# Optimization experiments

Measured on AMD Instinct MI355X. Metric: run time of the kernel, lower is better.

## Reference

```python
import jax, jax.numpy as jnp
import numpy as np

D = 1024      # config.input_dim
H = 16        # config.num_heads
EPS = 1e-6    # layernorm epsilon


def setup_inputs() -> dict:
    key = jax.random.key(0)
    ks = jax.random.split(key, 12)
    B, S = 4, 2048
    s = 1.0 / np.sqrt(D)
    return {
        "Q": jax.random.normal(ks[0], (B, S, D), jnp.float32),
        "K": jax.random.normal(ks[1], (B, S, D), jnp.float32),
        "V": jax.random.normal(ks[2], (B, S, D), jnp.float32),
        "Wq": jax.random.normal(ks[3], (D, D), jnp.float32) * s,
        "bq": jnp.zeros((D,), jnp.float32),
        "Wk": jax.random.normal(ks[4], (D, D), jnp.float32) * s,
        "bk": jnp.zeros((D,), jnp.float32),
        "Wv": jax.random.normal(ks[5], (D, D), jnp.float32) * s,
        "bv": jnp.zeros((D,), jnp.float32),
        "Wo": jax.random.normal(ks[6], (D, D), jnp.float32) * s,
        "bo": jnp.zeros((D,), jnp.float32),
        "gamma": jnp.ones((D,), jnp.float32),
        "beta": jnp.zeros((D,), jnp.float32),
    }


def _layernorm(x, gamma, beta):
    mu = jnp.mean(x, axis=-1, keepdims=True)
    var = jnp.mean(jnp.square(x - mu), axis=-1, keepdims=True)
    return (x - mu) * jax.lax.rsqrt(var + EPS) * gamma + beta


def reference(Q, K, V, Wq, bq, Wk, bk, Wv, bv, Wo, bo, gamma, beta):
    # Type == 'D': pre-norm projections, causal MHA (no 1/sqrt(d) scaling,
    # faithful to source), out projection, residual. Dropout = identity (eval).
    B, S, _ = Q.shape
    dh = D // H
    clone_Q = Q
    q = _layernorm(Q, gamma, beta) @ Wq + bq
    k = _layernorm(K, gamma, beta) @ Wk + bk
    v = _layernorm(V, gamma, beta) @ Wv + bv
    # [B, S, D] -> [B, H, S, dh]
    q = q.reshape(B, S, H, dh).transpose(0, 2, 1, 3)
    k = k.reshape(B, S, H, dh).transpose(0, 2, 1, 3)
    v = v.reshape(B, S, H, dh).transpose(0, 2, 1, 3)
    score = jnp.einsum("bhsd,bhtd->bhst", q, k)  # [B, H, S, S]
    causal = jnp.tril(jnp.ones((S, S), bool))
    score = jnp.where(causal, score, -jnp.inf)
    attn = jax.nn.softmax(score, axis=-1)
    out = jnp.einsum("bhst,bhtd->bhsd", attn, v)  # [B, H, S, dh]
    out = out.transpose(0, 2, 1, 3).reshape(B, S, D)
    return clone_Q + (out @ Wo + bo)
```

## Files before the change

kernel.cpp:

```cpp
#include <hip/hip_runtime.h>
#include <hip/hip_bf16.h>

typedef __attribute__((ext_vector_type(8))) __bf16 bf16x8;
typedef __attribute__((ext_vector_type(4))) float f32x4;

union BF8U { uint4 u; bf16x8 b; };

static __device__ __forceinline__ unsigned short f2bf(float f){
  __bf16 h = (__bf16)f;
  return *reinterpret_cast<unsigned short*>(&h);
}

static __device__ __forceinline__ bf16x8 ld_bf8(const unsigned short* p){
  BF8U u; u.u = *reinterpret_cast<const uint4*>(p); return u.b;
}

static __device__ __forceinline__ f32x4 mfma16(bf16x8 a, bf16x8 b, f32x4 c){
  return __builtin_amdgcn_mfma_f32_16x16x32_bf16(a, b, c, 0, 0, 0);
}

static __device__ __forceinline__ void gl_lds16(const unsigned short* g, unsigned short* l){
  __builtin_amdgcn_global_load_lds(
      (const __attribute__((address_space(1))) unsigned int*)g,
      (__attribute__((address_space(3))) unsigned int*)l, 16, 0, 0);
}

__global__ __launch_bounds__(256) void prep_kernel(
    const float* __restrict__ Q, const float* __restrict__ K, const float* __restrict__ V,
    const float* __restrict__ gamma, const float* __restrict__ beta,
    unsigned short* __restrict__ lnQ, unsigned short* __restrict__ lnK,
    unsigned short* __restrict__ lnV,
    const float* __restrict__ Wq, const float* __restrict__ Wk,
    const float* __restrict__ Wv, const float* __restrict__ Wo,
    unsigned short* __restrict__ WtQ, unsigned short* __restrict__ WtK,
    unsigned short* __restrict__ WtV, unsigned short* __restrict__ WtO)
{
  __shared__ __align__(16) unsigned short smem[64*72];
  const int bid = (int)blockIdx.x;
  const int t = threadIdx.x;
  if (bid < 24576){
    const int sel = bid >> 13;
    const int row = bid & 8191;
    const float* X = sel==0 ? Q : sel==1 ? K : V;
    unsigned short* out = sel==0 ? lnQ : sel==1 ? lnK : lnV;
    float* red = reinterpret_cast<float*>(smem);
    const float4 x = reinterpret_cast<const float4*>(X + (size_t)row*1024)[t];
    float s  = x.x + x.y + x.z + x.w;
    float ss = x.x*x.x + x.y*x.y + x.z*x.z + x.w*x.w;
    for (int off = 1; off < 64; off <<= 1){
      s  += __shfl_xor(s, off);
      ss += __shfl_xor(ss, off);
    }
    const int wv = t >> 6;
    if ((t & 63) == 0){ red[wv] = s; red[4 + wv] = ss; }
    __syncthreads();
    s  = red[0] + red[1] + red[2] + red[3];
    ss = red[4] + red[5] + red[6] + red[7];
    const float mu   = s * (1.0f/1024.0f);
    const float var  = ss * (1.0f/1024.0f) - mu*mu;
    const float rstd = rsqrtf(var + 1e-6f);
    const float4 gm = reinterpret_cast<const float4*>(gamma)[t];
    const float4 bt = reinterpret_cast<const float4*>(beta)[t];
    unsigned short pk[4];
    pk[0] = f2bf((x.x - mu)*rstd*gm.x + bt.x);
    pk[1] = f2bf((x.y - mu)*rstd*gm.y + bt.y);
    pk[2] = f2bf((x.z - mu)*rstd*gm.z + bt.z);
    pk[3] = f2bf((x.w - mu)*rstd*gm.w + bt.w);
    *reinterpret_cast<uint2*>(out + (size_t)row*1024 + t*4) = *reinterpret_cast<uint2*>(pk);
  } else {
    const int wid = bid - 24576;
    const int wsel = wid >> 8;
    const float* W = wsel==0 ? Wq : wsel==1 ? Wk : wsel==2 ? Wv : Wo;
    unsigned short* Wt = wsel==0 ? WtQ : wsel==1 ? WtK : wsel==2 ? WtV : WtO;
    unsigned short (*tile)[72] = reinterpret_cast<unsigned short(*)[72]>(smem);
    const int tb = wid & 255;
    const int bk = (tb >> 4) * 64;
    const int bn = (tb & 15) * 64;
    {
      const int kr = t >> 2, nc0 = (t & 3) * 16;
      const float4* src = reinterpret_cast<const float4*>(W + (size_t)(bk + kr)*1024 + bn + nc0);
      for (int q = 0; q < 4; ++q){
        float4 vv = src[q];
        tile[kr][nc0 + q*4 + 0] = f2bf(vv.x);
        tile[kr][nc0 + q*4 + 1] = f2bf(vv.y);
        tile[kr][nc0 + q*4 + 2] = f2bf(vv.z);
        tile[kr][nc0 + q*4 + 3] = f2bf(vv.w);
      }
    }
    __syncthreads();
    {
      const int nr = t >> 2, kc0 = (t & 3) * 16;
      unsigned short outv[16];
      for (int j = 0; j < 16; ++j) outv[j] = tile[kc0 + j][nr];
      uint4* dst = reinterpret_cast<uint4*>(Wt + (size_t)(bn + nr)*1024 + bk + kc0);
      dst[0] = reinterpret_cast<uint4*>(outv)[0];
      dst[1] = reinterpret_cast<uint4*>(outv)[1];
    }
  }
}

__global__ __launch_bounds__(256) void qkv_kernel(
    const unsigned short* __restrict__ lnQ, const unsigned short* __restrict__ lnK,
    const unsigned short* __restrict__ lnV,
    const unsigned short* __restrict__ WtQ, const unsigned short* __restrict__ WtK,
    const unsigned short* __restrict__ WtV,
    const float* __restrict__ bq, const float* __restrict__ bk,
    const float* __restrict__ bv,
    unsigned short* __restrict__ qb, unsigned short* __restrict__ kb,
    unsigned short* __restrict__ vtb)
{
  __shared__ unsigned short a_lds[128][64];
  __shared__ unsigned short b_lds[128][64];
  const int bid = (int)blockIdx.x;
  const int which = bid >> 9;
  const int inner = bid & 511;
  const unsigned short* A  = which==0 ? lnQ : which==1 ? lnK : lnV;
  const unsigned short* Bt = which==0 ? WtQ : which==1 ? WtK : WtV;
  const float* bias = which==0 ? bq : which==1 ? bk : bv;

  const int t = threadIdx.x;
  const int lane = t & 63;
  const int w = t >> 6;
  const int g = lane >> 4, c = lane & 15;
  const int bm = inner >> 3, bn = inner & 7;
  const int wr = w >> 1, wc = w & 1;
  const int row0 = bm * 128, col0 = bn * 128;

  f32x4 acc[4][4];
  const f32x4 fz = {0.f, 0.f, 0.f, 0.f};
  for (int i = 0; i < 4; ++i) for (int j = 0; j < 4; ++j) acc[i][j] = fz;

  for (int kb_ = 0; kb_ < 1024; kb_ += 64){
    for (int i = 0; i < 4; ++i){
      const int cid = t + i*256;
      const int r = cid >> 3, ch = cid & 7;
      const int chs = (ch ^ (r & 7)) * 8;
      gl_lds16(&A [(size_t)(row0 + r)*1024 + kb_ + chs], &a_lds[0][0] + cid*8);
      gl_lds16(&Bt[(size_t)(col0 + r)*1024 + kb_ + chs], &b_lds[0][0] + cid*8);
    }
    __syncthreads();
    bf16x8 af[4][2], bfr[4][2];
    for (int mt = 0; mt < 4; ++mt)
      for (int kc = 0; kc < 2; ++kc){
        const int R = wr*64 + mt*16 + c;
        af[mt][kc] = ld_bf8(&a_lds[R][((kc*4 + g) ^ (R & 7))*8]);
      }
    for (int nt = 0; nt < 4; ++nt)
      for (int kc = 0; kc < 2; ++kc){
        const int R = wc*64 + nt*16 + c;
        bfr[nt][kc] = ld_bf8(&b_lds[R][((kc*4 + g) ^ (R & 7))*8]);
      }
    for (int kc = 0; kc < 2; ++kc)
      for (int mt = 0; mt < 4; ++mt)
        for (int nt = 0; nt < 4; ++nt)
          acc[mt][nt] = mfma16(af[mt][kc], bfr[nt][kc], acc[mt][nt]);
    __syncthreads();
  }

  const float scale = (which == 0) ? 1.4426950408889634f : 1.0f;
  unsigned short* outb = which==0 ? qb : kb;
  for (int mt = 0; mt < 4; ++mt){
    for (int nt = 0; nt < 4; ++nt){
      const int gcol = col0 + wc*64 + nt*16 + c;
      const float bv_ = bias[gcol];
      const int hh = gcol >> 6, d = gcol & 63;
      if (which == 2){
        const int grow0 = row0 + wr*64 + mt*16 + g*4;
        const int bidx = grow0 >> 11, s0 = grow0 & 2047;
        unsigned short pk[4];
        for (int r = 0; r < 4; ++r) pk[r] = f2bf(acc[mt][nt][r] + bv_);
        *reinterpret_cast<uint2*>(&vtb[((size_t)((bidx*16 + hh)*64 + d))*2048 + s0]) =
          *reinterpret_cast<uint2*>(pk);
      } else {
        for (int r = 0; r < 4; ++r){
          const int grow = row0 + wr*64 + mt*16 + g*4 + r;
          const int bidx = grow >> 11, s = grow & 2047;
          outb[((size_t)(bidx*16 + hh)*2048 + s)*64 + d] = f2bf((acc[mt][nt][r] + bv_)*scale);
        }
      }
    }
  }
}

__global__ __launch_bounds__(256) void ogemm_kernel(
    const unsigned short* __restrict__ A,
    const unsigned short* __restrict__ Bt,
    const float* __restrict__ bias,
    const float* __restrict__ residual,
    float* __restrict__ outf)
{
  __shared__ unsigned short a_lds[128][64];
  __shared__ unsigned short b_lds[128][64];
  const int t = threadIdx.x;
  const int lane = t & 63;
  const int w = t >> 6;
  const int g = lane >> 4, c = lane & 15;
  const int bm = (int)blockIdx.x >> 3, bn = (int)blockIdx.x & 7;
  const int wr = w >> 1, wc = w & 1;
  const int row0 = bm * 128, col0 = bn * 128;

  f32x4 acc[4][4];
  const f32x4 fz = {0.f, 0.f, 0.f, 0.f};
  for (int i = 0; i < 4; ++i) for (int j = 0; j < 4; ++j) acc[i][j] = fz;

  for (int kb_ = 0; kb_ < 1024; kb_ += 64){
    for (int i = 0; i < 4; ++i){
      const int cid = t + i*256;
      const int r = cid >> 3, ch = cid & 7;
      const int chs = (ch ^ (r & 7)) * 8;
      gl_lds16(&A [(size_t)(row0 + r)*1024 + kb_ + chs], &a_lds[0][0] + cid*8);
      gl_lds16(&Bt[(size_t)(col0 + r)*1024 + kb_ + chs], &b_lds[0][0] + cid*8);
    }
    __syncthreads();
    bf16x8 af[4][2], bfr[4][2];
    for (int mt = 0; mt < 4; ++mt)
      for (int kc = 0; kc < 2; ++kc){
        const int R = wr*64 + mt*16 + c;
        af[mt][kc] = ld_bf8(&a_lds[R][((kc*4 + g) ^ (R & 7))*8]);
      }
    for (int nt = 0; nt < 4; ++nt)
      for (int kc = 0; kc < 2; ++kc){
        const int R = wc*64 + nt*16 + c;
        bfr[nt][kc] = ld_bf8(&b_lds[R][((kc*4 + g) ^ (R & 7))*8]);
      }
    for (int kc = 0; kc < 2; ++kc)
      for (int mt = 0; mt < 4; ++mt)
        for (int nt = 0; nt < 4; ++nt)
          acc[mt][nt] = mfma16(af[mt][kc], bfr[nt][kc], acc[mt][nt]);
    __syncthreads();
  }

  for (int mt = 0; mt < 4; ++mt){
    for (int nt = 0; nt < 4; ++nt){
      const int gcol = col0 + wc*64 + nt*16 + c;
      const float bv_ = bias[gcol];
      for (int r = 0; r < 4; ++r){
        const int grow = row0 + wr*64 + mt*16 + g*4 + r;
        const size_t idx = (size_t)grow*1024 + gcol;
        outf[idx] = acc[mt][nt][r] + bv_ + residual[idx];
      }
    }
  }
}

__global__ __launch_bounds__(512, 4) void attn_kernel(
    const unsigned short* __restrict__ qg,
    const unsigned short* __restrict__ kg,
    const unsigned short* __restrict__ vtg,
    unsigned short* __restrict__ og)
{
  __shared__ unsigned short k_lds[64][64];
  __shared__ unsigned short vt_lds[64][64];
  __shared__ unsigned short p_lds[8][16][72];
  const int t = threadIdx.x;
  const int lane = t & 63;
  const int w = t >> 6;
  const int g = lane >> 4, c = lane & 15;
  const int bh = (int)blockIdx.x & 63;
  const int p  = (int)blockIdx.x >> 6;
  const size_t base = (size_t)bh * 2048 * 64;
  const int bidx = bh >> 4, hh = bh & 15;
  const float NEG = -__builtin_inff();
  const f32x4 fz = {0.f,0.f,0.f,0.f};

  const int sr = t >> 3, sch = t & 7;
  const int schs = (sch ^ (sr & 7)) * 8;

  for (int half = 0; half < 2; ++half){
    const int qb_ = half ? (15 - p) : p;
    const int qw = qb_*128 + w*16;

    bf16x8 qf[2];
    for (int kc = 0; kc < 2; ++kc)
      qf[kc] = ld_bf8(&qg[base + (size_t)(qw + c)*64 + kc*32 + g*8]);

    f32x4 o_acc[4];
    for (int i = 0; i < 4; ++i) o_acc[i] = fz;
    float m_run = NEG, l_run = 0.f;

    const int nkv = qb_*2 + 2;
    for (int kvt = 0; kvt < nkv; ++kvt){
      const int kv0 = kvt * 64;
      gl_lds16(&kg [base + (size_t)(kv0 + sr)*64 + schs], &k_lds[0][0]  + t*8);
      gl_lds16(&vtg[base + (size_t)sr*2048 + kv0 + schs], &vt_lds[0][0] + t*8);
      __syncthreads();

      if (kv0 <= qw + 15){
        bf16x8 kf[4][2];
        for (int ni = 0; ni < 4; ++ni)
          for (int kc = 0; kc < 2; ++kc){
            const int R = ni*16 + c;
            kf[ni][kc] = ld_bf8(&k_lds[R][((kc*4 + g) ^ (R & 7))*8]);
          }
        f32x4 st[4];
        for (int i = 0; i < 4; ++i) st[i] = fz;
        __builtin_amdgcn_s_setprio(1);
        for (int kc = 0; kc < 2; ++kc)
          for (int ni = 0; ni < 4; ++ni)
            st[ni] = mfma16(kf[ni][kc], qf[kc], st[ni]);
        __builtin_amdgcn_s_setprio(0);

        const int qglob = qw + c;
        float tmax = NEG;
        if (kv0 + 63 > qw){
          for (int ni = 0; ni < 4; ++ni)
            for (int r = 0; r < 4; ++r){
              const int kvglob = kv0 + ni*16 + g*4 + r;
              float sv = (kvglob <= qglob) ? st[ni][r] : NEG;
              st[ni][r] = sv;
              tmax = fmaxf(tmax, sv);
            }
        } else {
          for (int ni = 0; ni < 4; ++ni)
            for (int r = 0; r < 4; ++r)
              tmax = fmaxf(tmax, st[ni][r]);
        }
        tmax = fmaxf(tmax, __shfl_xor(tmax, 16));
        tmax = fmaxf(tmax, __shfl_xor(tmax, 32));

        const bool defer = __all(tmax - m_run <= 11.5f);
        if (!defer){
          const float m_new = fmaxf(m_run, tmax);
          const float alpha = __builtin_amdgcn_exp2f(m_run - m_new);
          m_run = m_new;
          l_run *= alpha;
          for (int ni = 0; ni < 4; ++ni){
            o_acc[ni][0] *= alpha; o_acc[ni][1] *= alpha;
            o_acc[ni][2] *= alpha; o_acc[ni][3] *= alpha;
          }
        }
        float tsum = 0.f;
        for (int ni = 0; ni < 4; ++ni){
          unsigned short pk[4];
          for (int r = 0; r < 4; ++r){
            const float pe = __builtin_amdgcn_exp2f(st[ni][r] - m_run);
            tsum += pe;
            pk[r] = f2bf(pe);
          }
          *reinterpret_cast<uint2*>(&p_lds[w][c][ni*16 + g*4]) =
            *reinterpret_cast<uint2*>(pk);
        }
        tsum += __shfl_xor(tsum, 16);
        tsum += __shfl_xor(tsum, 32);
        l_run += tsum;

        bf16x8 vf[4][2], pf[2];
        for (int ni = 0; ni < 4; ++ni)
          for (int kc = 0; kc < 2; ++kc){
            const int R = ni*16 + c;
            vf[ni][kc] = ld_bf8(&vt_lds[R][((kc*4 + g) ^ (R & 7))*8]);
          }
        for (int kc = 0; kc < 2; ++kc)
          pf[kc] = ld_bf8(&p_lds[w][c][kc*32 + g*8]);
        __builtin_amdgcn_s_setprio(1);
        for (int kc = 0; kc < 2; ++kc)
          for (int ni = 0; ni < 4; ++ni)
            o_acc[ni] = mfma16(vf[ni][kc], pf[kc], o_acc[ni]);
        __builtin_amdgcn_s_setprio(0);
      }
      __syncthreads();
    }

    const float invl = 1.0f / l_run;
    const int s = qw + c;
    const size_t obase = ((size_t)(bidx*2048 + s))*1024 + hh*64;
    for (int ni = 0; ni < 4; ++ni){
      unsigned short pk[4];
      pk[0] = f2bf(o_acc[ni][0]*invl);
      pk[1] = f2bf(o_acc[ni][1]*invl);
      pk[2] = f2bf(o_acc[ni][2]*invl);
      pk[3] = f2bf(o_acc[ni][3]*invl);
      *reinterpret_cast<uint2*>(&og[obase + ni*16 + g*4]) =
        *reinterpret_cast<uint2*>(pk);
    }
  }
}

extern "C" void kernel_launch(void* const* d_in, const int* in_sizes, int n_in,
                              void* d_out, int out_size, void* d_ws, size_t ws_size,
                              hipStream_t stream)
{
  (void)in_sizes; (void)n_in; (void)out_size;
  const float* Q  = (const float*)d_in[0];
  const float* K  = (const float*)d_in[1];
  const float* V  = (const float*)d_in[2];
  const float* Wq = (const float*)d_in[3];
  const float* bq = (const float*)d_in[4];
  const float* Wk = (const float*)d_in[5];
  const float* bk = (const float*)d_in[6];
  const float* Wv = (const float*)d_in[7];
  const float* bv = (const float*)d_in[8];
  const float* Wo = (const float*)d_in[9];
  const float* bo = (const float*)d_in[10];
  const float* gamma = (const float*)d_in[11];
  const float* beta  = (const float*)d_in[12];

  const size_t MB = 1024ull*1024ull;
  if (ws_size < 104*MB) return;
  char* ws = (char*)d_ws;
  unsigned short* lnQ = (unsigned short*)(ws + 0*MB);
  unsigned short* lnK = (unsigned short*)(ws + 16*MB);
  unsigned short* lnV = (unsigned short*)(ws + 32*MB);
  unsigned short* attn_out = lnQ;
  unsigned short* WtQ = (unsigned short*)(ws + 48*MB);
  unsigned short* WtK = (unsigned short*)(ws + 50*MB);
  unsigned short* WtV = (unsigned short*)(ws + 52*MB);
  unsigned short* WtO = (unsigned short*)(ws + 54*MB);
  unsigned short* qb  = (unsigned short*)(ws + 56*MB);
  unsigned short* kb  = (unsigned short*)(ws + 72*MB);
  unsigned short* vtb = (unsigned short*)(ws + 88*MB);
  float* out = (float*)d_out;

  prep_kernel<<<25600, 256, 0, stream>>>(Q, K, V, gamma, beta, lnQ, lnK, lnV,
                                         Wq, Wk, Wv, Wo, WtQ, WtK, WtV, WtO);
  qkv_kernel<<<1536, 256, 0, stream>>>(lnQ, lnK, lnV, WtQ, WtK, WtV,
                                       bq, bk, bv, qb, kb, vtb);
  attn_kernel<<<512, 512, 0, stream>>>(qb, kb, vtb, attn_out);
  ogemm_kernel<<<512, 256, 0, stream>>>(attn_out, WtO, bo, Q, out);
}
```

Before: 336.9 us.

## Use per-wave layernorm rows, swizzle GEMM block order, compute softmax denominator via MFMA

```diff
diff --git a/kernel.cpp b/kernel.cpp
--- a/kernel.cpp
+++ b/kernel.cpp
@@ -35,44 +35,47 @@
     unsigned short* __restrict__ WtQ, unsigned short* __restrict__ WtK,
     unsigned short* __restrict__ WtV, unsigned short* __restrict__ WtO)
 {
-  __shared__ __align__(16) unsigned short smem[64*72];
   const int bid = (int)blockIdx.x;
   const int t = threadIdx.x;
-  if (bid < 24576){
-    const int sel = bid >> 13;
-    const int row = bid & 8191;
+  if (bid < 6144){
+    const int row = bid*4 + (t >> 6);
+    const int lane = t & 63;
+    const int sel = row >> 13;
+    const int r0 = row & 8191;
     const float* X = sel==0 ? Q : sel==1 ? K : V;
     unsigned short* out = sel==0 ? lnQ : sel==1 ? lnK : lnV;
-    float* red = reinterpret_cast<float*>(smem);
-    const float4 x = reinterpret_cast<const float4*>(X + (size_t)row*1024)[t];
-    float s  = x.x + x.y + x.z + x.w;
-    float ss = x.x*x.x + x.y*x.y + x.z*x.z + x.w*x.w;
+    const float4* xp = reinterpret_cast<const float4*>(X + (size_t)r0*1024);
+    float4 xv[4];
+    float s = 0.f, ss = 0.f;
+    for (int i = 0; i < 4; ++i){
+      xv[i] = xp[lane + i*64];
+      s  += xv[i].x + xv[i].y + xv[i].z + xv[i].w;
+      ss += xv[i].x*xv[i].x + xv[i].y*xv[i].y + xv[i].z*xv[i].z + xv[i].w*xv[i].w;
+    }
     for (int off = 1; off < 64; off <<= 1){
       s  += __shfl_xor(s, off);
       ss += __shfl_xor(ss, off);
     }
-    const int wv = t >> 6;
-    if ((t & 63) == 0){ red[wv] = s; red[4 + wv] = ss; }
-    __syncthreads();
-    s  = red[0] + red[1] + red[2] + red[3];
-    ss = red[4] + red[5] + red[6] + red[7];
     const float mu   = s * (1.0f/1024.0f);
     const float var  = ss * (1.0f/1024.0f) - mu*mu;
     const float rstd = rsqrtf(var + 1e-6f);
-    const float4 gm = reinterpret_cast<const float4*>(gamma)[t];
-    const float4 bt = reinterpret_cast<const float4*>(beta)[t];
-    unsigned short pk[4];
-    pk[0] = f2bf((x.x - mu)*rstd*gm.x + bt.x);
-    pk[1] = f2bf((x.y - mu)*rstd*gm.y + bt.y);
-    pk[2] = f2bf((x.z - mu)*rstd*gm.z + bt.z);
-    pk[3] = f2bf((x.w - mu)*rstd*gm.w + bt.w);
-    *reinterpret_cast<uint2*>(out + (size_t)row*1024 + t*4) = *reinterpret_cast<uint2*>(pk);
+    for (int i = 0; i < 4; ++i){
+      const float4 gm = reinterpret_cast<const float4*>(gamma)[lane + i*64];
+      const float4 bt = reinterpret_cast<const float4*>(beta )[lane + i*64];
+      unsigned short pk[4];
+      pk[0] = f2bf((xv[i].x - mu)*rstd*gm.x + bt.x);
+      pk[1] = f2bf((xv[i].y - mu)*rstd*gm.y + bt.y);
+      pk[2] = f2bf((xv[i].z - mu)*rstd*gm.z + bt.z);
+      pk[3] = f2bf((xv[i].w - mu)*rstd*gm.w + bt.w);
+      *reinterpret_cast<uint2*>(out + (size_t)r0*1024 + (lane + i*64)*4) =
+        *reinterpret_cast<uint2*>(pk);
+    }
   } else {
-    const int wid = bid - 24576;
+    __shared__ unsigned short tile[64][72];
+    const int wid = bid - 6144;
     const int wsel = wid >> 8;
     const float* W = wsel==0 ? Wq : wsel==1 ? Wk : wsel==2 ? Wv : Wo;
     unsigned short* Wt = wsel==0 ? WtQ : wsel==1 ? WtK : wsel==2 ? WtV : WtO;
-    unsigned short (*tile)[72] = reinterpret_cast<unsigned short(*)[72]>(smem);
     const int tb = wid & 255;
     const int bk = (tb >> 4) * 64;
     const int bn = (tb & 15) * 64;
@@ -114,6 +117,7 @@
   const int bid = (int)blockIdx.x;
   const int which = bid >> 9;
   const int inner = bid & 511;
+  const int swz = ((inner & 7) << 6) | (inner >> 3);
   const unsigned short* A  = which==0 ? lnQ : which==1 ? lnK : lnV;
   const unsigned short* Bt = which==0 ? WtQ : which==1 ? WtK : WtV;
   const float* bias = which==0 ? bq : which==1 ? bk : bv;
@@ -122,7 +126,7 @@
   const int lane = t & 63;
   const int w = t >> 6;
   const int g = lane >> 4, c = lane & 15;
-  const int bm = inner >> 3, bn = inner & 7;
+  const int bm = swz >> 3, bn = swz & 7;
   const int wr = w >> 1, wc = w & 1;
   const int row0 = bm * 128, col0 = bn * 128;
 
@@ -192,10 +196,12 @@
   __shared__ unsigned short a_lds[128][64];
   __shared__ unsigned short b_lds[128][64];
   const int t = threadIdx.x;
+  const int inner = (int)blockIdx.x;
+  const int swz = ((inner & 7) << 6) | (inner >> 3);
   const int lane = t & 63;
   const int w = t >> 6;
   const int g = lane >> 4, c = lane & 15;
-  const int bm = (int)blockIdx.x >> 3, bn = (int)blockIdx.x & 7;
+  const int bm = swz >> 3, bn = swz & 7;
   const int wr = w >> 1, wc = w & 1;
   const int row0 = bm * 128, col0 = bn * 128;
 
@@ -262,6 +268,8 @@
   const int bidx = bh >> 4, hh = bh & 15;
   const float NEG = -__builtin_inff();
   const f32x4 fz = {0.f,0.f,0.f,0.f};
+  BF8U onesu; onesu.u = make_uint4(0x3F803F80u,0x3F803F80u,0x3F803F80u,0x3F803F80u);
+  const bf16x8 ones = onesu.b;
 
   const int sr = t >> 3, sch = t & 7;
   const int schs = (sch ^ (sr & 7)) * 8;
@@ -276,7 +284,8 @@
 
     f32x4 o_acc[4];
     for (int i = 0; i < 4; ++i) o_acc[i] = fz;
-    float m_run = NEG, l_run = 0.f;
+    f32x4 l_acc = fz;
+    float m_run = NEG;
 
     const int nkv = qb_*2 + 2;
     for (int kvt = 0; kvt < nkv; ++kvt){
@@ -323,26 +332,19 @@
           const float m_new = fmaxf(m_run, tmax);
           const float alpha = __builtin_amdgcn_exp2f(m_run - m_new);
           m_run = m_new;
-          l_run *= alpha;
+          l_acc[0] *= alpha;
           for (int ni = 0; ni < 4; ++ni){
             o_acc[ni][0] *= alpha; o_acc[ni][1] *= alpha;
             o_acc[ni][2] *= alpha; o_acc[ni][3] *= alpha;
           }
         }
-        float tsum = 0.f;
         for (int ni = 0; ni < 4; ++ni){
           unsigned short pk[4];
-          for (int r = 0; r < 4; ++r){
-            const float pe = __builtin_amdgcn_exp2f(st[ni][r] - m_run);
-            tsum += pe;
-            pk[r] = f2bf(pe);
-          }
+          for (int r = 0; r < 4; ++r)
+            pk[r] = f2bf(__builtin_amdgcn_exp2f(st[ni][r] - m_run));
           *reinterpret_cast<uint2*>(&p_lds[w][c][ni*16 + g*4]) =
             *reinterpret_cast<uint2*>(pk);
         }
-        tsum += __shfl_xor(tsum, 16);
-        tsum += __shfl_xor(tsum, 32);
-        l_run += tsum;
 
         bf16x8 vf[4][2], pf[2];
         for (int ni = 0; ni < 4; ++ni)
@@ -353,6 +355,8 @@
         for (int kc = 0; kc < 2; ++kc)
           pf[kc] = ld_bf8(&p_lds[w][c][kc*32 + g*8]);
         __builtin_amdgcn_s_setprio(1);
+        l_acc = mfma16(ones, pf[0], l_acc);
+        l_acc = mfma16(ones, pf[1], l_acc);
         for (int kc = 0; kc < 2; ++kc)
           for (int ni = 0; ni < 4; ++ni)
             o_acc[ni] = mfma16(vf[ni][kc], pf[kc], o_acc[ni]);
@@ -361,7 +365,7 @@
       __syncthreads();
     }
 
-    const float invl = 1.0f / l_run;
+    const float invl = 1.0f / l_acc[0];
     const int s = qw + c;
     const size_t obase = ((size_t)(bidx*2048 + s))*1024 + hh*64;
     for (int ni = 0; ni < 4; ++ni){
@@ -411,8 +415,8 @@
   unsigned short* vtb = (unsigned short*)(ws + 88*MB);
   float* out = (float*)d_out;
 
-  prep_kernel<<<25600, 256, 0, stream>>>(Q, K, V, gamma, beta, lnQ, lnK, lnV,
-                                         Wq, Wk, Wv, Wo, WtQ, WtK, WtV, WtO);
+  prep_kernel<<<7168, 256, 0, stream>>>(Q, K, V, gamma, beta, lnQ, lnK, lnV,
+                                        Wq, Wk, Wv, Wo, WtQ, WtK, WtV, WtO);
   qkv_kernel<<<1536, 256, 0, stream>>>(lnQ, lnK, lnV, WtQ, WtK, WtV,
                                        bq, bk, bv, qb, kb, vtb);
   attn_kernel<<<512, 512, 0, stream>>>(qb, kb, vtb, attn_out);
```

Result: faster. 314.4 us (-6.7%).
